# Performance work log

Measured on AMD Instinct MI355X. Metric: run time of the kernel, lower is better.

The kernel has to match this reference:

```python
import jax, jax.numpy as jnp
import numpy as np

N_E = 8192
E_DIM = 64
BETA = 0.25
N_TOKENS = 32768


def setup_inputs() -> dict:
    key = jax.random.key(0)
    k1, k2 = jax.random.split(key)
    x = jax.random.normal(k1, (N_TOKENS, E_DIM), dtype=jnp.float32)
    # nn.Embedding weight initialized uniform(-1/n_e, 1/n_e)
    codebook = jax.random.uniform(k2, (N_E, E_DIM), dtype=jnp.float32,
                                  minval=-1.0 / N_E, maxval=1.0 / N_E)
    return {"x": x, "codebook": codebook, "start": 0, "end": N_E, "use_sk": 0}


def reference(x, codebook, start, end, use_sk):
    # use_sk=0 -> argmin branch (sinkhorn branch calls external helper, not exercised)
    latent = x.reshape(-1, E_DIM)                       # [N, D]
    cb = codebook[start:end]                            # [K, D]
    # squared euclidean distances: ||z||^2 + ||e||^2 - 2 z.e
    d = (jnp.sum(latent * latent, axis=1, keepdims=True)
         + jnp.sum(cb * cb, axis=1)[None, :]
         - 2.0 * jnp.einsum('nd,kd->nk', latent, cb))   # [N, K]
    indices = jnp.argmin(d, axis=-1) + start            # [N]
    x_q = codebook[indices].reshape(x.shape)            # gather
    sg = jax.lax.stop_gradient
    commitment_loss = jnp.mean((sg(x_q) - x) ** 2)
    codebook_loss = jnp.mean((x_q - sg(x)) ** 2)
    loss = codebook_loss + BETA * commitment_loss
    x_q_st = x + sg(x_q - x)                            # straight-through estimator
    indices = indices.reshape(x.shape[:-1])
    return x_q_st, loss, indices
```

## Files before the change

### kernel.cpp

```cpp
#include <hip/hip_runtime.h>
#include <math.h>


#define N_E    8192
#define EDIM   64
#define NTOK   32768
#define NELEM  (NTOK * EDIM)
#define CSZ    32
#define NCHUNK (N_E / CSZ)
#define WINDOW 3e-4f
#define KEXT   80
#define TTOK   256
#define TCODE  2048
#define SROW   88

typedef __attribute__((ext_vector_type(8)))  short          short8;
typedef __attribute__((ext_vector_type(8)))  unsigned short ushort8v;
typedef __attribute__((ext_vector_type(4)))  unsigned short ushort4v;
typedef __attribute__((ext_vector_type(16))) float          f32x16;

__device__ __forceinline__ unsigned short f2bf(float f) {
  unsigned int u = __float_as_uint(f);
  return (unsigned short)((u + 0x7FFFu + ((u >> 16) & 1u)) >> 16);
}
__device__ __forceinline__ unsigned short f2h(float f) {
  union { _Float16 h; unsigned short u; } cv; cv.h = (_Float16)f; return cv.u;
}
__device__ __forceinline__ float h2f(unsigned short b) {
  union { _Float16 h; unsigned short u; } cv; cv.u = b; return (float)cv.h;
}

__global__ __launch_bounds__(256) void vq_sc(const float* __restrict__ cb,
                                             float* __restrict__ sc,
                                             unsigned short* __restrict__ cbf) {
#pragma clang fp contract(off)
  int r = blockIdx.x * 256 + threadIdx.x;
  const float4* c4 = (const float4*)(cb + (size_t)r * EDIM);
  float a[8];
#pragma unroll
  for (int j = 0; j < 8; ++j) a[j] = 0.0f;
#pragma unroll
  for (int i = 0; i < 8; ++i) {
    float4 pA = c4[2*i], pB = c4[2*i+1];
    a[0] += pA.x * pA.x; a[1] += pA.y * pA.y; a[2] += pA.z * pA.z; a[3] += pA.w * pA.w;
    a[4] += pB.x * pB.x; a[5] += pB.y * pB.y; a[6] += pB.z * pB.z; a[7] += pB.w * pB.w;
  }
  float sval = ((a[0]+a[1]) + (a[2]+a[3])) + ((a[4]+a[5]) + (a[6]+a[7]));
  sc[r] = sval;
  unsigned short* dst = cbf + (size_t)r * KEXT;
#pragma unroll
  for (int h = 0; h < 8; ++h) {
    float4 fA = c4[2*h], fB = c4[2*h+1];
    ushort8v o = {f2bf(fA.x), f2bf(fA.y), f2bf(fA.z), f2bf(fA.w),
                  f2bf(fB.x), f2bf(fB.y), f2bf(fB.z), f2bf(fB.w)};
    *(ushort8v*)&dst[h * 8] = o;
  }
  ushort8v t0 = {0,0,0,0,0,0,0,0};
  t0[0] = f2bf(sval);
  *(ushort8v*)&dst[64] = t0;
  ushort8v z = {0,0,0,0,0,0,0,0};
  *(ushort8v*)&dst[72] = z;
}

__global__ __launch_bounds__(256, 2) void vq_pass1(
    const float* __restrict__ x, const unsigned short* __restrict__ cbf,
    unsigned short* __restrict__ minima, unsigned int* __restrict__ maskb,
    const int* __restrict__ p_start, const int* __restrict__ p_end) {
  __shared__ unsigned short Xs[TTOK * SROW];
  __shared__ unsigned short Cs[128 * SROW];
  int tid = threadIdx.x;
  int tb = blockIdx.x;
  int cbk = blockIdx.y;
  int s = *p_start, e = *p_end;

  const float4* xg = (const float4*)(x + (size_t)tb * TTOK * EDIM);
#pragma unroll
  for (int p = 0; p < 16; ++p) {
    int idx = tid + p * 256;
    int row = idx >> 4, c4i = idx & 15;
    float4 f = xg[idx];
    ushort4v o = {f2bf(f.x), f2bf(f.y), f2bf(f.z), f2bf(f.w)};
    *(ushort4v*)&Xs[row * SROW + c4i * 4] = o;
  }
  {
    ushort8v t0 = {0,0,0,0,0,0,0,0};
    t0[0] = f2bf(-0.5f);
    ushort8v z = {0,0,0,0,0,0,0,0};
    *(ushort8v*)&Xs[tid * SROW + 64] = t0;
    *(ushort8v*)&Xs[tid * SROW + 72] = z;
  }
  const ushort8v* cg0 = (const ushort8v*)(cbf + (size_t)cbk * TCODE * KEXT);
#pragma unroll
  for (int p = 0; p < 5; ++p) {
    int idx = tid + p * 256;
    int row = idx / 10, h = idx % 10;
    *(ushort8v*)&Cs[row * SROW + h * 8] = cg0[idx];
  }
  __syncthreads();

  int lane = tid & 63, wv = tid >> 6;
  int half = lane >> 5, ln = lane & 31;
  int tokbase = wv * 64;
  short8 bfr[2][5];
#pragma unroll
  for (int tg = 0; tg < 2; ++tg)
#pragma unroll
    for (int ks = 0; ks < 5; ++ks)
      bfr[tg][ks] = *(const short8*)&Xs[(tokbase + tg*32 + ln) * SROW + ks*16 + half*8];

  for (int nb = 0; nb < 16; ++nb) {
    ushort8v creg[5];
    if (nb < 15) {
      const ushort8v* cg =
          (const ushort8v*)(cbf + ((size_t)cbk * TCODE + (nb + 1) * 128) * KEXT);
#pragma unroll
      for (int p = 0; p < 5; ++p) creg[p] = cg[tid + p * 256];
    }
    f32x16 acc[2][4];
#pragma unroll
    for (int tg = 0; tg < 2; ++tg)
#pragma unroll
      for (int ct = 0; ct < 4; ++ct) acc[tg][ct] = (f32x16)0.0f;
#pragma unroll
    for (int ks = 0; ks < 5; ++ks)
#pragma unroll
      for (int ct = 0; ct < 4; ++ct) {
        short8 a = *(const short8*)&Cs[(ct*32 + ln) * SROW + ks*16 + half*8];
        acc[0][ct] = __builtin_amdgcn_mfma_f32_32x32x16_bf16(a, bfr[0][ks],
                                                             acc[0][ct], 0, 0, 0);
        acc[1][ct] = __builtin_amdgcn_mfma_f32_32x32x16_bf16(a, bfr[1][ks],
                                                             acc[1][ct], 0, 0, 0);
      }
    __syncthreads();
    if (nb < 15) {
#pragma unroll
      for (int p = 0; p < 5; ++p) {
        int idx = tid + p * 256;
        int row = idx / 10, h = idx % 10;
        *(ushort8v*)&Cs[row * SROW + h * 8] = creg[p];
      }
    }
    int cbase0 = cbk * TCODE + nb * 128;
    float vmv[2][4];
    unsigned mbits[2][4];
#pragma unroll
    for (int ct = 0; ct < 4; ++ct) {
      int c0 = cbase0 + ct * 32;
      bool full = (c0 >= s) && (c0 + 32 <= e);
#pragma unroll
      for (int tg = 0; tg < 2; ++tg) {
        float v = -INFINITY;
        if (full) {
#pragma unroll
          for (int r = 0; r < 16; ++r) v = fmaxf(v, acc[tg][ct][r]);
        } else {
#pragma unroll
          for (int r = 0; r < 16; ++r) {
            int code = c0 + (r & 3) + 8 * (r >> 2) + 4 * half;
            if (code >= s && code < e) v = fmaxf(v, acc[tg][ct][r]);
          }
        }
        v = fmaxf(v, __shfl_xor(v, 32, 64));
        vmv[tg][ct] = v;
        float t = v - WINDOW * 0.5f;
        unsigned b = 0;
#pragma unroll
        for (int r = 0; r < 16; ++r) {
          int pos = (r & 3) + 8 * (r >> 2) + 4 * half;
          if (acc[tg][ct][r] >= t) b |= (1u << pos);
        }
        b |= __shfl_xor(b, 32, 64);
        mbits[tg][ct] = b;
      }
    }
    int token = tb * TTOK + tokbase + lane;
    uint2 pk;
    pk.x = (unsigned int)f2h(-2.0f * vmv[half][0])
         | ((unsigned int)f2h(-2.0f * vmv[half][1]) << 16);
    pk.y = (unsigned int)f2h(-2.0f * vmv[half][2])
         | ((unsigned int)f2h(-2.0f * vmv[half][3]) << 16);
    *(uint2*)(minima + (size_t)token * NCHUNK + (cbase0 >> 5)) = pk;
    uint4 mq;
    mq.x = mbits[half][0]; mq.y = mbits[half][1];
    mq.z = mbits[half][2]; mq.w = mbits[half][3];
    *(uint4*)(maskb + (size_t)token * NCHUNK + (cbase0 >> 5)) = mq;
    __syncthreads();
  }
}

__global__ __launch_bounds__(256) void vq_rescue(
    const float* __restrict__ x, const float* __restrict__ cb,
    const float* __restrict__ sc, const unsigned short* __restrict__ minima,
    const unsigned int* __restrict__ maskb,
    float* __restrict__ out_xq, float* __restrict__ out_idx,
    float* __restrict__ partial,
    const int* __restrict__ p_start, const int* __restrict__ p_end) {
#pragma clang fp contract(off)
  __shared__ float xs[4][64];
  __shared__ float sdata[4];
  int tid  = threadIdx.x;
  int wv   = tid >> 6;
  int lane = tid & 63;
  int token = blockIdx.x * 4 + wv;

  float xx = x[(size_t)token * EDIM + lane];
  xs[wv][lane] = xx;
  __syncthreads();
  const float4* xl4 = (const float4*)xs[wv];

  float a[8];
#pragma unroll
  for (int j = 0; j < 8; ++j) a[j] = 0.0f;
#pragma unroll
  for (int i = 0; i < 8; ++i) {
    float4 pA = xl4[2*i], pB = xl4[2*i+1];
    a[0] += pA.x * pA.x; a[1] += pA.y * pA.y; a[2] += pA.z * pA.z; a[3] += pA.w * pA.w;
    a[4] += pB.x * pB.x; a[5] += pB.y * pB.y; a[6] += pB.z * pB.z; a[7] += pB.w * pB.w;
  }
  float sx = ((a[0]+a[1]) + (a[2]+a[3])) + ((a[4]+a[5]) + (a[6]+a[7]));

  uint2 u2 = *(const uint2*)(minima + (size_t)token * NCHUNK + lane * 4);
  float mv[4] = {h2f((unsigned short)(u2.x & 0xFFFFu)),
                 h2f((unsigned short)(u2.x >> 16)),
                 h2f((unsigned short)(u2.y & 0xFFFFu)),
                 h2f((unsigned short)(u2.y >> 16))};
  float m = fminf(fminf(mv[0], mv[1]), fminf(mv[2], mv[3]));
#pragma unroll
  for (int off = 32; off >= 1; off >>= 1) m = fminf(m, __shfl_xor(m, off, 64));
  float thr = m + WINDOW;

  int s = *p_start, e = *p_end;
  unsigned long long bestpack = ~0ull;

  bool anyf = (mv[0] <= thr) | (mv[1] <= thr) | (mv[2] <= thr) | (mv[3] <= thr);
  if (anyf) {
    uint4 mq = *(const uint4*)(maskb + (size_t)token * NCHUNK + lane * 4);
    unsigned mks[4] = {mq.x, mq.y, mq.z, mq.w};
#pragma unroll 1
    for (int cc = 0; cc < 4; ++cc) {
      if (!(mv[cc] <= thr)) continue;
      unsigned msk = mks[cc];
      while (msk) {
        int j = __ffs(msk) - 1;
        msk &= msk - 1;
        int k = (lane * 4 + cc) * CSZ + j;
        if (k >= s && k < e) {
          const float4* c4 = (const float4*)(cb + (size_t)k * EDIM);
          float t[8];
#pragma unroll
          for (int jj = 0; jj < 8; ++jj) t[jj] = 0.0f;
#pragma unroll
          for (int i = 0; i < 8; ++i) {
            float4 cA4 = c4[2*i], cB4 = c4[2*i+1];
            float4 pA = xl4[2*i], pB = xl4[2*i+1];
            t[0] += cA4.x * pA.x; t[1] += cA4.y * pA.y;
            t[2] += cA4.z * pA.z; t[3] += cA4.w * pA.w;
            t[4] += cB4.x * pB.x; t[5] += cB4.y * pB.y;
            t[6] += cB4.z * pB.z; t[7] += cB4.w * pB.w;
          }
          float tt = ((t[0]+t[1]) + (t[2]+t[3])) + ((t[4]+t[5]) + (t[6]+t[7]));
          float d = (sx + sc[k]) - 2.0f * tt;
          unsigned int db = __float_as_uint(d);
          unsigned int en = db ^ ((unsigned int)((int)db >> 31) | 0x80000000u);
          unsigned long long pk = ((unsigned long long)en << 32) | (unsigned int)k;
          if (pk < bestpack) bestpack = pk;
        }
      }
    }
  }
#pragma unroll
  for (int off = 32; off >= 1; off >>= 1) {
    unsigned long long o = __shfl_xor(bestpack, off, 64);
    if (o < bestpack) bestpack = o;
  }
  int bidx = (int)(unsigned int)(bestpack & 0xFFFFFFFFull);

  float qv = cb[(size_t)bidx * EDIM + lane];
  float diff = qv - xx;
  out_xq[(size_t)token * EDIM + lane] = xx + diff;
  if (lane == 0) out_idx[token] = (float)bidx;

  float l = diff * diff;
#pragma unroll
  for (int off = 32; off >= 1; off >>= 1) l += __shfl_down(l, off, 64);
  if (lane == 0) sdata[wv] = l;
  __syncthreads();
  if (tid == 0)
    partial[blockIdx.x] = (sdata[0] + sdata[1]) + (sdata[2] + sdata[3]);
}

__global__ __launch_bounds__(256) void vq_loss(const float* __restrict__ partial,
                                               float* __restrict__ out_loss) {
  int tid = threadIdx.x;
  float s = 0.0f;
  for (int i = tid; i < NTOK / 4; i += 256) s += partial[i];
#pragma unroll
  for (int off = 32; off >= 1; off >>= 1) s += __shfl_down(s, off, 64);
  __shared__ float sdata[4];
  if ((tid & 63) == 0) sdata[tid >> 6] = s;
  __syncthreads();
  if (tid == 0) {
    float total = (sdata[0] + sdata[1]) + (sdata[2] + sdata[3]);
    float m = total * (1.0f / (float)NELEM);
    out_loss[0] = m + 0.25f * m;
  }
}

extern "C" void kernel_launch(void* const* d_in, const int* in_sizes, int n_in,
                              void* d_out, int out_size, void* d_ws, size_t ws_size,
                              hipStream_t stream) {
  const float* x  = (const float*)d_in[0];
  const float* cb = (const float*)d_in[1];
  const int* p_start = (const int*)d_in[2];
  const int* p_end   = (const int*)d_in[3];

  float* ws = (float*)d_ws;
  float* sc      = ws;
  float* partial = ws + N_E;
  unsigned short* cbf    = (unsigned short*)(ws + 2 * N_E);
  unsigned short* minima = cbf + (size_t)N_E * KEXT;
  unsigned int*   maskb  = (unsigned int*)(minima + (size_t)NTOK * NCHUNK);

  float* out      = (float*)d_out;
  float* out_xq   = out;
  float* out_loss = out + NELEM;
  float* out_idx  = out + NELEM + 1;

  vq_sc<<<N_E / 256, 256, 0, stream>>>(cb, sc, cbf);
  dim3 g1(NTOK / TTOK, N_E / TCODE);
  vq_pass1<<<g1, 256, 0, stream>>>(x, cbf, minima, maskb, p_start, p_end);
  vq_rescue<<<NTOK / 4, 256, 0, stream>>>(x, cb, sc, minima, maskb, out_xq, out_idx,
                                          partial, p_start, p_end);
  vq_loss<<<1, 256, 0, stream>>>(partial, out_loss);
}
```

Before: 213.2 us.

## Drop augmented norm column, stage minima in LDS, rescue whole chunks via ballot

The codebook norm column is removed from the bf16 MFMA operands, cutting the K dimension from 80 to 64. Per-chunk candidate values now skip the codebook norm, which holds only because the codebook norms are tiny. X is converted straight into registers instead of going through shared memory. Per-token chunk minima are staged in LDS and written out with coalesced 16-byte stores, and the per-code mask buffer is removed. The rescue kernel uses a ballot over candidate chunks and evaluates all 32 codes of two chunks per wave in parallel. This trades fewer pass-1 writes and less divergence for more exact distance evaluations in rescue.

```diff
diff --git a/kernel.cpp b/kernel.cpp
--- a/kernel.cpp
+++ b/kernel.cpp
@@ -9,14 +9,13 @@
 #define CSZ    32
 #define NCHUNK (N_E / CSZ)
 #define WINDOW 3e-4f
-#define KEXT   80
 #define TTOK   256
 #define TCODE  2048
-#define SROW   88
+#define SROW   72
+#define MROW   72
 
 typedef __attribute__((ext_vector_type(8)))  short          short8;
 typedef __attribute__((ext_vector_type(8)))  unsigned short ushort8v;
-typedef __attribute__((ext_vector_type(4)))  unsigned short ushort4v;
 typedef __attribute__((ext_vector_type(16))) float          f32x16;
 
 __device__ __forceinline__ unsigned short f2bf(float f) {
@@ -28,6 +27,13 @@
 }
 __device__ __forceinline__ float h2f(unsigned short b) {
   union { _Float16 h; unsigned short u; } cv; cv.u = b; return (float)cv.h;
+}
+__device__ __forceinline__ float max16(const f32x16 a) {
+  float m0 = fmaxf(fmaxf(a[0], a[1]),   fmaxf(a[2], a[3]));
+  float m1 = fmaxf(fmaxf(a[4], a[5]),   fmaxf(a[6], a[7]));
+  float m2 = fmaxf(fmaxf(a[8], a[9]),   fmaxf(a[10], a[11]));
+  float m3 = fmaxf(fmaxf(a[12], a[13]), fmaxf(a[14], a[15]));
+  return fmaxf(fmaxf(m0, m1), fmaxf(m2, m3));
 }
 
 __global__ __launch_bounds__(256) void vq_sc(const float* __restrict__ cb,
@@ -47,7 +53,7 @@
   }
   float sval = ((a[0]+a[1]) + (a[2]+a[3])) + ((a[4]+a[5]) + (a[6]+a[7]));
   sc[r] = sval;
-  unsigned short* dst = cbf + (size_t)r * KEXT;
+  unsigned short* dst = cbf + (size_t)r * EDIM;
 #pragma unroll
   for (int h = 0; h < 8; ++h) {
     float4 fA = c4[2*h], fB = c4[2*h+1];
@@ -55,66 +61,55 @@
                   f2bf(fB.x), f2bf(fB.y), f2bf(fB.z), f2bf(fB.w)};
     *(ushort8v*)&dst[h * 8] = o;
   }
-  ushort8v t0 = {0,0,0,0,0,0,0,0};
-  t0[0] = f2bf(sval);
-  *(ushort8v*)&dst[64] = t0;
-  ushort8v z = {0,0,0,0,0,0,0,0};
-  *(ushort8v*)&dst[72] = z;
 }
 
 __global__ __launch_bounds__(256, 2) void vq_pass1(
     const float* __restrict__ x, const unsigned short* __restrict__ cbf,
-    unsigned short* __restrict__ minima, unsigned int* __restrict__ maskb,
+    unsigned short* __restrict__ minima,
     const int* __restrict__ p_start, const int* __restrict__ p_end) {
-  __shared__ unsigned short Xs[TTOK * SROW];
   __shared__ unsigned short Cs[128 * SROW];
+  __shared__ unsigned short minL[TTOK * MROW];
   int tid = threadIdx.x;
   int tb = blockIdx.x;
   int cbk = blockIdx.y;
   int s = *p_start, e = *p_end;
 
-  const float4* xg = (const float4*)(x + (size_t)tb * TTOK * EDIM);
-#pragma unroll
-  for (int p = 0; p < 16; ++p) {
-    int idx = tid + p * 256;
-    int row = idx >> 4, c4i = idx & 15;
-    float4 f = xg[idx];
-    ushort4v o = {f2bf(f.x), f2bf(f.y), f2bf(f.z), f2bf(f.w)};
-    *(ushort4v*)&Xs[row * SROW + c4i * 4] = o;
-  }
-  {
-    ushort8v t0 = {0,0,0,0,0,0,0,0};
-    t0[0] = f2bf(-0.5f);
-    ushort8v z = {0,0,0,0,0,0,0,0};
-    *(ushort8v*)&Xs[tid * SROW + 64] = t0;
-    *(ushort8v*)&Xs[tid * SROW + 72] = z;
-  }
-  const ushort8v* cg0 = (const ushort8v*)(cbf + (size_t)cbk * TCODE * KEXT);
-#pragma unroll
-  for (int p = 0; p < 5; ++p) {
-    int idx = tid + p * 256;
-    int row = idx / 10, h = idx % 10;
-    *(ushort8v*)&Cs[row * SROW + h * 8] = cg0[idx];
-  }
-  __syncthreads();
-
   int lane = tid & 63, wv = tid >> 6;
   int half = lane >> 5, ln = lane & 31;
   int tokbase = wv * 64;
-  short8 bfr[2][5];
-#pragma unroll
-  for (int tg = 0; tg < 2; ++tg)
-#pragma unroll
-    for (int ks = 0; ks < 5; ++ks)
-      bfr[tg][ks] = *(const short8*)&Xs[(tokbase + tg*32 + ln) * SROW + ks*16 + half*8];
+
+  const ushort8v* cg0 = (const ushort8v*)(cbf + (size_t)cbk * TCODE * EDIM);
+#pragma unroll
+  for (int p = 0; p < 4; ++p) {
+    int idx = tid + p * 256;
+    int row = idx >> 3, h = idx & 7;
+    *(ushort8v*)&Cs[row * SROW + h * 8] = cg0[idx];
+  }
+
+  short8 bfr[2][4];
+#pragma unroll
+  for (int tg = 0; tg < 2; ++tg) {
+    const float* xrow =
+        x + (size_t)(tb * TTOK + tokbase + tg * 32 + ln) * EDIM + half * 8;
+#pragma unroll
+    for (int ks = 0; ks < 4; ++ks) {
+      float4 fA = *(const float4*)(xrow + ks * 16);
+      float4 fB = *(const float4*)(xrow + ks * 16 + 4);
+      short8 v = {(short)f2bf(fA.x), (short)f2bf(fA.y), (short)f2bf(fA.z),
+                  (short)f2bf(fA.w), (short)f2bf(fB.x), (short)f2bf(fB.y),
+                  (short)f2bf(fB.z), (short)f2bf(fB.w)};
+      bfr[tg][ks] = v;
+    }
+  }
+  __syncthreads();
 
   for (int nb = 0; nb < 16; ++nb) {
-    ushort8v creg[5];
+    ushort8v creg[4];
     if (nb < 15) {
       const ushort8v* cg =
-          (const ushort8v*)(cbf + ((size_t)cbk * TCODE + (nb + 1) * 128) * KEXT);
-#pragma unroll
-      for (int p = 0; p < 5; ++p) creg[p] = cg[tid + p * 256];
+          (const ushort8v*)(cbf + ((size_t)cbk * TCODE + (nb + 1) * 128) * EDIM);
+#pragma unroll
+      for (int p = 0; p < 4; ++p) creg[p] = cg[tid + p * 256];
     }
     f32x16 acc[2][4];
 #pragma unroll
@@ -122,7 +117,7 @@
 #pragma unroll
       for (int ct = 0; ct < 4; ++ct) acc[tg][ct] = (f32x16)0.0f;
 #pragma unroll
-    for (int ks = 0; ks < 5; ++ks)
+    for (int ks = 0; ks < 4; ++ks)
 #pragma unroll
       for (int ct = 0; ct < 4; ++ct) {
         short8 a = *(const short8*)&Cs[(ct*32 + ln) * SROW + ks*16 + half*8];
@@ -134,64 +129,57 @@
     __syncthreads();
     if (nb < 15) {
 #pragma unroll
-      for (int p = 0; p < 5; ++p) {
+      for (int p = 0; p < 4; ++p) {
         int idx = tid + p * 256;
-        int row = idx / 10, h = idx % 10;
+        int row = idx >> 3, h = idx & 7;
         *(ushort8v*)&Cs[row * SROW + h * 8] = creg[p];
       }
     }
     int cbase0 = cbk * TCODE + nb * 128;
-    float vmv[2][4];
-    unsigned mbits[2][4];
+    unsigned int hsel[4];
 #pragma unroll
     for (int ct = 0; ct < 4; ++ct) {
       int c0 = cbase0 + ct * 32;
       bool full = (c0 >= s) && (c0 + 32 <= e);
-#pragma unroll
-      for (int tg = 0; tg < 2; ++tg) {
-        float v = -INFINITY;
-        if (full) {
-#pragma unroll
-          for (int r = 0; r < 16; ++r) v = fmaxf(v, acc[tg][ct][r]);
-        } else {
-#pragma unroll
-          for (int r = 0; r < 16; ++r) {
-            int code = c0 + (r & 3) + 8 * (r >> 2) + 4 * half;
-            if (code >= s && code < e) v = fmaxf(v, acc[tg][ct][r]);
+      float v0, v1;
+      if (full) {
+        v0 = max16(acc[0][ct]);
+        v1 = max16(acc[1][ct]);
+      } else {
+        v0 = -INFINITY; v1 = -INFINITY;
+#pragma unroll
+        for (int r = 0; r < 16; ++r) {
+          int code = c0 + (r & 3) + 8 * (r >> 2) + 4 * half;
+          if (code >= s && code < e) {
+            v0 = fmaxf(v0, acc[0][ct][r]);
+            v1 = fmaxf(v1, acc[1][ct][r]);
           }
         }
-        v = fmaxf(v, __shfl_xor(v, 32, 64));
-        vmv[tg][ct] = v;
-        float t = v - WINDOW * 0.5f;
-        unsigned b = 0;
-#pragma unroll
-        for (int r = 0; r < 16; ++r) {
-          int pos = (r & 3) + 8 * (r >> 2) + 4 * half;
-          if (acc[tg][ct][r] >= t) b |= (1u << pos);
-        }
-        b |= __shfl_xor(b, 32, 64);
-        mbits[tg][ct] = b;
       }
-    }
-    int token = tb * TTOK + tokbase + lane;
+      v0 = fmaxf(v0, __shfl_xor(v0, 32, 64));
+      v1 = fmaxf(v1, __shfl_xor(v1, 32, 64));
+      float vs = half ? v1 : v0;
+      hsel[ct] = (unsigned int)f2h(-2.0f * vs);
+    }
     uint2 pk;
-    pk.x = (unsigned int)f2h(-2.0f * vmv[half][0])
-         | ((unsigned int)f2h(-2.0f * vmv[half][1]) << 16);
-    pk.y = (unsigned int)f2h(-2.0f * vmv[half][2])
-         | ((unsigned int)f2h(-2.0f * vmv[half][3]) << 16);
-    *(uint2*)(minima + (size_t)token * NCHUNK + (cbase0 >> 5)) = pk;
-    uint4 mq;
-    mq.x = mbits[half][0]; mq.y = mbits[half][1];
-    mq.z = mbits[half][2]; mq.w = mbits[half][3];
-    *(uint4*)(maskb + (size_t)token * NCHUNK + (cbase0 >> 5)) = mq;
+    pk.x = hsel[0] | (hsel[1] << 16);
+    pk.y = hsel[2] | (hsel[3] << 16);
+    *(uint2*)&minL[(unsigned)tid * MROW + nb * 4] = pk;
     __syncthreads();
+  }
+
+#pragma unroll
+  for (int p = 0; p < 8; ++p) {
+    int idx = tid + p * 256;
+    int tl = idx >> 3, part = idx & 7;
+    uint4 v = *(const uint4*)&minL[tl * MROW + part * 8];
+    *(uint4*)(minima + ((size_t)(tb * TTOK + tl)) * NCHUNK + cbk * 64 + part * 8) = v;
   }
 }
 
 __global__ __launch_bounds__(256) void vq_rescue(
     const float* __restrict__ x, const float* __restrict__ cb,
     const float* __restrict__ sc, const unsigned short* __restrict__ minima,
-    const unsigned int* __restrict__ maskb,
     float* __restrict__ out_xq, float* __restrict__ out_idx,
     float* __restrict__ partial,
     const int* __restrict__ p_start, const int* __restrict__ p_end) {
@@ -231,19 +219,18 @@
 
   int s = *p_start, e = *p_end;
   unsigned long long bestpack = ~0ull;
-
-  bool anyf = (mv[0] <= thr) | (mv[1] <= thr) | (mv[2] <= thr) | (mv[3] <= thr);
-  if (anyf) {
-    uint4 mq = *(const uint4*)(maskb + (size_t)token * NCHUNK + lane * 4);
-    unsigned mks[4] = {mq.x, mq.y, mq.z, mq.w};
-#pragma unroll 1
-    for (int cc = 0; cc < 4; ++cc) {
-      if (!(mv[cc] <= thr)) continue;
-      unsigned msk = mks[cc];
-      while (msk) {
-        int j = __ffs(msk) - 1;
-        msk &= msk - 1;
-        int k = (lane * 4 + cc) * CSZ + j;
+  int ln32 = lane & 31;
+
+#pragma unroll
+  for (int cc = 0; cc < 4; ++cc) {
+    unsigned long long bal = __ballot(mv[cc] <= thr);
+    while (bal) {
+      int l0 = __ffsll(bal) - 1; bal &= bal - 1;
+      int l1 = -1;
+      if (bal) { l1 = __ffsll(bal) - 1; bal &= bal - 1; }
+      int lsel = (lane < 32) ? l0 : l1;
+      if (lsel >= 0) {
+        int k = (lsel * 4 + cc) * CSZ + ln32;
         if (k >= s && k < e) {
           const float4* c4 = (const float4*)(cb + (size_t)k * EDIM);
           float t[8];
@@ -318,8 +305,7 @@
   float* sc      = ws;
   float* partial = ws + N_E;
   unsigned short* cbf    = (unsigned short*)(ws + 2 * N_E);
-  unsigned short* minima = cbf + (size_t)N_E * KEXT;
-  unsigned int*   maskb  = (unsigned int*)(minima + (size_t)NTOK * NCHUNK);
+  unsigned short* minima = cbf + (size_t)N_E * EDIM;
 
   float* out      = (float*)d_out;
   float* out_xq   = out;
@@ -328,8 +314,8 @@
 
   vq_sc<<<N_E / 256, 256, 0, stream>>>(cb, sc, cbf);
   dim3 g1(NTOK / TTOK, N_E / TCODE);
-  vq_pass1<<<g1, 256, 0, stream>>>(x, cbf, minima, maskb, p_start, p_end);
-  vq_rescue<<<NTOK / 4, 256, 0, stream>>>(x, cb, sc, minima, maskb, out_xq, out_idx,
+  vq_pass1<<<g1, 256, 0, stream>>>(x, cbf, minima, p_start, p_end);
+  vq_rescue<<<NTOK / 4, 256, 0, stream>>>(x, cb, sc, minima, out_xq, out_idx,
                                           partial, p_start, p_end);
   vq_loss<<<1, 256, 0, stream>>>(partial, out_loss);
 }
```

New measurement: 229.9 us. 1.08x slower.
